# Performance work log

Hardware: AMD Instinct MI355X
Metric: run time of the kernel (lower is better)

## Reference

```python
import jax, jax.numpy as jnp
import numpy as np

# Standard NF4 quantization codebook (bitsandbytes values)
_NF4_CB = np.array([
    -1.0, -0.6961928009986877, -0.5250730514526367, -0.39491748809814453,
    -0.28444138169288635, -0.18477343022823334, -0.09105003625154495, 0.0,
    0.07958029955625534, 0.16093020141124725, 0.24611230194568634, 0.33791524171829224,
    0.44070982933044434, 0.5626170039176941, 0.7229568362236023, 1.0], dtype=np.float32)

B, L, H, E, DFF = 2, 2048, 2048, 8, 8192
BLK = 512  # NF4 quantization block size (b_idx = h // 512 in kernel)


def setup_inputs() -> dict:
    key = jax.random.key(0)
    ks = jax.random.split(key, 8)
    N = B * L
    x = jax.random.normal(ks[0], (B, L, H), dtype=jnp.float32)
    router_w = jax.random.normal(ks[1], (H, E), dtype=jnp.float32) * 0.02
    # packed NF4: one byte = two 4-bit codebook indices (low nibble -> even h)
    nf4 = jax.random.randint(ks[2], (N, E, H // 2), 0, 256, dtype=jnp.int32)
    mean = jax.random.normal(ks[3], (N, E, H // BLK), dtype=jnp.float32) * 0.01
    std = jax.random.uniform(ks[4], (N, E, H // BLK), dtype=jnp.float32) + 0.5
    codebook = jnp.asarray(_NF4_CB)
    w1 = jax.random.normal(ks[5], (H, DFF), dtype=jnp.float32) * 0.02
    w2 = jax.random.normal(ks[6], (DFF, H), dtype=jnp.float32) * 0.02
    return {"x": x, "router_w": router_w, "nf4": nf4, "mean": mean,
            "std": std, "codebook": codebook, "w1": w1, "w2": w2}


def reference(x, router_w, nf4, mean, std, codebook, w1, w2):
    b, l, h = x.shape
    n = b * l
    e = router_w.shape[1]
    xf = x.reshape(n, h)

    # shared expert MLP (base_mlp): Linear -> GELU -> Linear
    mlp = jax.nn.gelu(xf @ w1) @ w2  # [N, H]

    # router: logits in fp32, softmax, cast to fp16 as the kernel does
    logits = xf @ router_w  # [N, E]
    probs = jax.nn.softmax(logits, axis=-1).astype(jnp.float16).astype(jnp.float32)

    # NF4 unpack: low nibble -> even h, high nibble -> odd h
    low = nf4 & 15
    high = (nf4 >> 4) & 15
    idx = jnp.stack([low, high], axis=-1).reshape(n, e, h)  # interleave -> [N,E,H]
    vals = codebook[idx]  # codebook gather, [N,E,H]

    # per-block (512) rescale: val*std + mean
    nb = mean.shape[-1]
    blk = h // nb
    dq = (vals.reshape(n, e, nb, blk) * std[..., None] + mean[..., None]).reshape(n, e, h)

    # weighted expert mix + MLP residual add
    moe = jnp.einsum('ne,neh->nh', probs, dq)
    return (moe + mlp).reshape(b, l, h)
```

## Files before the change

### kernel.cpp

```cpp
#include <hip/hip_runtime.h>
#include <hip/hip_bf16.h>
#include <hip/hip_fp16.h>

#define H 2048
#define E 8
#define DFF 8192
#define NTOK 4096
#define NB 4

typedef _Float16 f16x8 __attribute__((ext_vector_type(8)));
typedef _Float16 f16x2 __attribute__((ext_vector_type(2)));
typedef float f32x4 __attribute__((ext_vector_type(4)));

#define AS1 __attribute__((address_space(1)))
#define AS3 __attribute__((address_space(3)))

__device__ __forceinline__ void gl_lds16(const void* g, void* l) {
    __builtin_amdgcn_global_load_lds((const AS1 unsigned int*)g,
                                     (AS3 unsigned int*)l, 16, 0, 0);
}

__device__ __forceinline__ float gelu_f(float x) {
    float u = 0.7978845608028654f * x * (1.0f + 0.044715f * x * x);
    float t = fabsf(u);
    float e = __expf(-2.0f * t);
    float th = (1.0f - e) / (1.0f + e);
    th = copysignf(th, u);
    return 0.5f * x * (1.0f + th);
}

__global__ __launch_bounds__(256) void router_moe_kernel(
    const float* __restrict__ x, const float* __restrict__ rw,
    const int* __restrict__ nf4, const float* __restrict__ mean,
    const float* __restrict__ stdv, const float* __restrict__ cb,
    _Float16* __restrict__ xh, float* __restrict__ moe)
{
    int n = blockIdx.x, t = threadIdx.x;
    __shared__ float red[4][E];
    __shared__ float pr[E];
    __shared__ float cbl[32];
    __shared__ float ps[E][NB];
    __shared__ float cmean[NB];

    float acc[E];
#pragma unroll
    for (int e = 0; e < E; ++e) acc[e] = 0.f;
    const float* xr = x + (size_t)n * H;
#pragma unroll
    for (int k = 0; k < H / 256; ++k) {
        int h = t + k * 256;
        float xv = xr[h];
        xh[(size_t)n * H + h] = (_Float16)xv;
        const float4* r4 = reinterpret_cast<const float4*>(rw + (size_t)h * E);
        float4 a = r4[0], b = r4[1];
        acc[0] += xv * a.x; acc[1] += xv * a.y; acc[2] += xv * a.z; acc[3] += xv * a.w;
        acc[4] += xv * b.x; acc[5] += xv * b.y; acc[6] += xv * b.z; acc[7] += xv * b.w;
    }
#pragma unroll
    for (int e = 0; e < E; ++e) {
        float v = acc[e];
#pragma unroll
        for (int o = 32; o > 0; o >>= 1) v += __shfl_down(v, o, 64);
        acc[e] = v;
    }
    int wave = t >> 6, lane = t & 63;
    if (lane == 0) {
#pragma unroll
        for (int e = 0; e < E; ++e) red[wave][e] = acc[e];
    }
    __syncthreads();
    if (t == 0) {
        float lg[E];
        float mx = -1e30f;
#pragma unroll
        for (int e = 0; e < E; ++e) {
            lg[e] = red[0][e] + red[1][e] + red[2][e] + red[3][e];
            mx = fmaxf(mx, lg[e]);
        }
        float s = 0.f;
#pragma unroll
        for (int e = 0; e < E; ++e) { lg[e] = expf(lg[e] - mx); s += lg[e]; }
        float inv = 1.f / s;
#pragma unroll
        for (int e = 0; e < E; ++e) {
            float p = lg[e] * inv;
            pr[e] = __half2float(__float2half(p));
        }
    }
    __syncthreads();

    if (t < 16) { float v = cb[t]; cbl[t] = v; cbl[t + 16] = v; }
    else if (t >= 32 && t < 64) {
        int e = (t - 32) >> 2, b = t & 3;
        ps[e][b] = pr[e] * stdv[((size_t)n * E + e) * NB + b];
    } else if (t >= 64 && t < 68) {
        int b = t - 64; float s = 0.f;
        for (int e = 0; e < E; ++e)
            s += pr[e] * mean[((size_t)n * E + e) * NB + b];
        cmean[b] = s;
    }
    __syncthreads();

    int b = t >> 6;
    int cboff = (t & 1) << 4;
    const int4* w4 = reinterpret_cast<const int4*>(nf4 + (size_t)n * (E * H / 2));
    float o[8];
    float cm = cmean[b];
#pragma unroll
    for (int u = 0; u < 8; ++u) o[u] = cm;
#pragma unroll
    for (int e = 0; e < E; ++e) {
        int4 wv = w4[e * 256 + t];
        float pse = ps[e][b];
        int w0 = wv.x, w1 = wv.y, w2 = wv.z, w3 = wv.w;
        o[0] += pse * cbl[(w0 & 15) + cboff];
        o[1] += pse * cbl[((w0 >> 4) & 15) + cboff];
        o[2] += pse * cbl[(w1 & 15) + cboff];
        o[3] += pse * cbl[((w1 >> 4) & 15) + cboff];
        o[4] += pse * cbl[(w2 & 15) + cboff];
        o[5] += pse * cbl[((w2 >> 4) & 15) + cboff];
        o[6] += pse * cbl[(w3 & 15) + cboff];
        o[7] += pse * cbl[((w3 >> 4) & 15) + cboff];
    }
    float4* op = reinterpret_cast<float4*>(moe + (size_t)n * H + 8 * t);
    op[0] = make_float4(o[0], o[1], o[2], o[3]);
    op[1] = make_float4(o[4], o[5], o[6], o[7]);
}

__global__ __launch_bounds__(256) void transpose_cast_kernel(
    const float* __restrict__ src, _Float16* __restrict__ dst, int R, int C)
{
    __shared__ float tile[64][65];
    int t = threadIdx.x;
    int c0 = blockIdx.x * 64, r0 = blockIdx.y * 64;
    int ct = (t & 15) * 4, rt = t >> 4;
#pragma unroll
    for (int i = 0; i < 4; ++i) {
        int r = rt + i * 16;
        float4 v = *reinterpret_cast<const float4*>(src + (size_t)(r0 + r) * C + c0 + ct);
        tile[r][ct] = v.x; tile[r][ct + 1] = v.y;
        tile[r][ct + 2] = v.z; tile[r][ct + 3] = v.w;
    }
    __syncthreads();
    int u = (t & 31) * 2, cq = t >> 5;
#pragma unroll
    for (int i = 0; i < 8; ++i) {
        int c = cq + i * 8;
        f16x2 pk;
        pk[0] = (_Float16)tile[u][c];
        pk[1] = (_Float16)tile[u + 1][c];
        *reinterpret_cast<f16x2*>(dst + (size_t)(c0 + c) * R + r0 + u) = pk;
    }
}

template <int EPI, int MAP>
__global__ __launch_bounds__(512, 2) void gemm5b_kernel(
    const _Float16* __restrict__ A, const _Float16* __restrict__ Bt,
    const float* __restrict__ addsrc, void* __restrict__ outv,
    float* __restrict__ aux, int K, int LDK, int N)
{
    __shared__ uint4 lds_u4[163840 / 16];
    char* lds = (char*)lds_u4;

    int t = threadIdx.x;
    int id = blockIdx.x;
    int xcd = id & 7, chunk = id >> 3;
    int by, bx, ks = 0;
    if constexpr (MAP == 0) {
        by = (xcd & 1) * 8 + (chunk & 7);
        bx = (xcd >> 1) * 8 + (chunk >> 3);
    } else {
        by = (xcd >> 1) * 4 + (chunk & 3);
        bx = (xcd & 1) * 4 + ((chunk >> 2) & 3);
        ks = chunk >> 4;
    }
    int m0 = by * 256, n0 = bx * 256;
    int koff = ks * K;

    const unsigned short* sA = (const unsigned short*)A
        + (size_t)(m0 + (t & 255)) * LDK + koff + (t >> 8) * 8;
    const unsigned short* sB = (const unsigned short*)Bt
        + (size_t)(n0 + (t & 255)) * LDK + koff + (t >> 8) * 8;
    unsigned dstT = (unsigned)t * 16;

    int lane = t & 63, wave = t >> 6;
    int wr = wave >> 2, wc = wave & 3;
    int mb = wr * 128, nb = wc * 64;
    int q = lane >> 4, m16 = lane & 15;

    unsigned aOff = (unsigned)(q * 4096 + (mb + m16) * 16);
    unsigned bOff = (unsigned)(16384 + q * 4096 + (nb + m16) * 16);

    f32x4 acc[8][4] = {};
    f16x8 afL[4], afH[4], bf[4];

#define STG_A(Wb, T) do { \
    gl_lds16(sA + (size_t)(T) * 32,      (Wb) + dstT); \
    gl_lds16(sA + (size_t)(T) * 32 + 16, (Wb) + 8192 + dstT); } while (0)
#define STG_B(Wb, T) do { \
    gl_lds16(sB + (size_t)(T) * 32,      (Wb) + 16384 + dstT); \
    gl_lds16(sB + (size_t)(T) * 32 + 16, (Wb) + 16384 + 8192 + dstT); } while (0)
#define RD_B(Rb) do { \
    _Pragma("unroll") for (int jl = 0; jl < 4; ++jl) \
        bf[jl] = *(const f16x8*)((Rb) + bOff + jl * 256); } while (0)
#define RD_AL(Rb) do { \
    _Pragma("unroll") for (int il = 0; il < 4; ++il) \
        afL[il] = *(const f16x8*)((Rb) + aOff + il * 256); } while (0)
#define RD_AH(Rb) do { \
    _Pragma("unroll") for (int il = 0; il < 4; ++il) \
        afH[il] = *(const f16x8*)((Rb) + aOff + 1024 + il * 256); } while (0)
#define MM(i0, afr) do { \
    __builtin_amdgcn_s_setprio(1); \
    _Pragma("unroll") for (int il = 0; il < 4; ++il) \
    _Pragma("unroll") for (int jl = 0; jl < 4; ++jl) \
        acc[(i0) + il][jl] = __builtin_amdgcn_mfma_f32_16x16x32_f16( \
            afr[il], bf[jl], acc[(i0) + il][jl], 0, 0, 0); \
    __builtin_amdgcn_s_setprio(0); } while (0)
#define BARR  asm volatile("s_barrier" ::: "memory")
#define LGKM0 asm volatile("s_waitcnt lgkmcnt(0)" ::: "memory")

    STG_A(lds,         0); STG_B(lds,         0);
    STG_A(lds + 32768, 1); STG_B(lds + 32768, 1);
    STG_A(lds + 65536, 2); STG_B(lds + 65536, 2);
    asm volatile("s_waitcnt vmcnt(8)" ::: "memory");
    BARR;

    int NT = K / 32;
    unsigned rb = 0, wb = 3 * 32768;
    for (int T = 0; T < NT; ++T) {
        char* R = lds + rb;
        char* W = lds + wb;
        bool st = (T + 3 < NT);

        RD_B(R); RD_AL(R);
        if (st) STG_A(W, T + 3);
        BARR; LGKM0;
        MM(0, afL);
        BARR;
        RD_AH(R);
        if (st) STG_B(W, T + 3);
        BARR; LGKM0;
        MM(4, afH);
        if (st) asm volatile("s_waitcnt vmcnt(8)" ::: "memory");
        else    asm volatile("s_waitcnt vmcnt(0)" ::: "memory");
        BARR;

        rb += 32768; if (rb == 163840) rb = 0;
        wb += 32768; if (wb == 163840) wb = 0;
    }

#pragma unroll
    for (int i = 0; i < 8; ++i)
#pragma unroll
        for (int j = 0; j < 4; ++j) {
            int row = m0 + mb + i * 16 + q * 4;
            int col = n0 + nb + j * 16 + m16;
#pragma unroll
            for (int rix = 0; rix < 4; ++rix) {
                float v = acc[i][j][rix];
                size_t o = (size_t)(row + rix) * N + col;
                if constexpr (EPI == 0) {
                    ((_Float16*)outv)[o] = (_Float16)gelu_f(v);
                } else {
                    if (ks == 0) ((float*)outv)[o] = v + addsrc[o];
                    else         aux[o] = v;
                }
            }
        }
#undef STG_A
#undef STG_B
#undef RD_B
#undef RD_AL
#undef RD_AH
#undef MM
#undef BARR
#undef LGKM0
}

__global__ __launch_bounds__(256) void combine_kernel(
    float* __restrict__ out, const float* __restrict__ part)
{
    size_t base = (size_t)blockIdx.x * 256 + threadIdx.x;
    const float4* p4 = (const float4*)part;
    float4* o4 = (float4*)out;
#pragma unroll
    for (int s = 0; s < 4; ++s) {
        size_t i = base + (size_t)s * 524288;
        float4 a = o4[i], b = p4[i];
        o4[i] = make_float4(a.x + b.x, a.y + b.y, a.z + b.z, a.w + b.w);
    }
}

extern "C" void kernel_launch(void* const* d_in, const int* in_sizes, int n_in,
                              void* d_out, int out_size, void* d_ws, size_t ws_size,
                              hipStream_t stream) {
    const float* x    = (const float*)d_in[0];
    const float* rw   = (const float*)d_in[1];
    const int*   nf4  = (const int*)d_in[2];
    const float* mean = (const float*)d_in[3];
    const float* stdv = (const float*)d_in[4];
    const float* cb   = (const float*)d_in[5];
    const float* w1   = (const float*)d_in[6];
    const float* w2   = (const float*)d_in[7];
    float* out = (float*)d_out;

    char* ws = (char*)d_ws;
    float* moe        = (float*)(ws + 131072);
    _Float16* xh      = (_Float16*)(ws + 33685504);
    _Float16* w1t     = (_Float16*)(ws + 50462720);
    _Float16* w2t     = (_Float16*)(ws + 84017152);
    _Float16* hid     = (_Float16*)(ws + 117571584);
    float* pbuf       = (float*)(ws + 50462720);

    router_moe_kernel<<<NTOK, 256, 0, stream>>>(x, rw, nf4, mean, stdv, cb, xh, moe);
    transpose_cast_kernel<<<dim3(DFF / 64, H / 64), 256, 0, stream>>>(w1, w1t, H, DFF);
    transpose_cast_kernel<<<dim3(H / 64, DFF / 64), 256, 0, stream>>>(w2, w2t, DFF, H);
    gemm5b_kernel<0, 0><<<512, 512, 0, stream>>>(xh, w1t, nullptr, (void*)hid,
                                                 nullptr, H, H, DFF);
    gemm5b_kernel<1, 1><<<256, 512, 0, stream>>>(hid, w2t, moe, (void*)out,
                                                 pbuf, DFF / 2, DFF, H);
    combine_kernel<<<2048, 256, 0, stream>>>(out, pbuf);
}
```

Before: 724.8 us.

## Drop mid-iteration GEMM barriers and merge the two weight-transpose launches

The GEMM main loop loses its two mid-iteration s_barrier and lgkmcnt(0) waits and the s_setprio toggles around the MFMA blocks. Both A and B staging for tile T+3 are now issued up front, leaving one barrier per K-step; the 5-slot LDS ring keeps the read and write slots apart. The two transpose-cast launches are folded into one kernel that picks w1 or w2 by block index. The goal is less barrier stall and launch overhead, at the cost of letting waves drift apart and possibly worse MFMA/memory interleaving without the priority hints.

```diff
diff --git a/kernel.cpp b/kernel.cpp
--- a/kernel.cpp
+++ b/kernel.cpp
@@ -127,12 +127,23 @@
     op[1] = make_float4(o[4], o[5], o[6], o[7]);
 }
 
-__global__ __launch_bounds__(256) void transpose_cast_kernel(
-    const float* __restrict__ src, _Float16* __restrict__ dst, int R, int C)
+__global__ __launch_bounds__(256) void transpose2_kernel(
+    const float* __restrict__ w1, const float* __restrict__ w2,
+    _Float16* __restrict__ w1t, _Float16* __restrict__ w2t)
 {
     __shared__ float tile[64][65];
+    int id = blockIdx.x;
+    const float* src; _Float16* dst; int R, C, bx, by;
+    if (id < (DFF / 64) * (H / 64)) {
+        src = w1; dst = w1t; R = H; C = DFF;
+        bx = id % (DFF / 64); by = id / (DFF / 64);
+    } else {
+        id -= (DFF / 64) * (H / 64);
+        src = w2; dst = w2t; R = DFF; C = H;
+        bx = id % (H / 64); by = id / (H / 64);
+    }
     int t = threadIdx.x;
-    int c0 = blockIdx.x * 64, r0 = blockIdx.y * 64;
+    int c0 = bx * 64, r0 = by * 64;
     int ct = (t & 15) * 4, rt = t >> 4;
 #pragma unroll
     for (int i = 0; i < 4; ++i) {
@@ -154,7 +165,7 @@
 }
 
 template <int EPI, int MAP>
-__global__ __launch_bounds__(512, 2) void gemm5b_kernel(
+__global__ __launch_bounds__(512, 2) void gemmW_kernel(
     const _Float16* __restrict__ A, const _Float16* __restrict__ Bt,
     const float* __restrict__ addsrc, void* __restrict__ outv,
     float* __restrict__ aux, int K, int LDK, int N)
@@ -210,14 +221,11 @@
     _Pragma("unroll") for (int il = 0; il < 4; ++il) \
         afH[il] = *(const f16x8*)((Rb) + aOff + 1024 + il * 256); } while (0)
 #define MM(i0, afr) do { \
-    __builtin_amdgcn_s_setprio(1); \
     _Pragma("unroll") for (int il = 0; il < 4; ++il) \
     _Pragma("unroll") for (int jl = 0; jl < 4; ++jl) \
         acc[(i0) + il][jl] = __builtin_amdgcn_mfma_f32_16x16x32_f16( \
-            afr[il], bf[jl], acc[(i0) + il][jl], 0, 0, 0); \
-    __builtin_amdgcn_s_setprio(0); } while (0)
+            afr[il], bf[jl], acc[(i0) + il][jl], 0, 0, 0); } while (0)
 #define BARR  asm volatile("s_barrier" ::: "memory")
-#define LGKM0 asm volatile("s_waitcnt lgkmcnt(0)" ::: "memory")
 
     STG_A(lds,         0); STG_B(lds,         0);
     STG_A(lds + 32768, 1); STG_B(lds + 32768, 1);
@@ -232,15 +240,13 @@
         char* W = lds + wb;
         bool st = (T + 3 < NT);
 
-        RD_B(R); RD_AL(R);
-        if (st) STG_A(W, T + 3);
-        BARR; LGKM0;
+        RD_B(R);
+        RD_AL(R);
+        if (st) { STG_A(W, T + 3); STG_B(W, T + 3); }
         MM(0, afL);
-        BARR;
         RD_AH(R);
-        if (st) STG_B(W, T + 3);
-        BARR; LGKM0;
         MM(4, afH);
+
         if (st) asm volatile("s_waitcnt vmcnt(8)" ::: "memory");
         else    asm volatile("s_waitcnt vmcnt(0)" ::: "memory");
         BARR;
@@ -274,7 +280,6 @@
 #undef RD_AH
 #undef MM
 #undef BARR
-#undef LGKM0
 }
 
 __global__ __launch_bounds__(256) void combine_kernel(
@@ -313,11 +318,10 @@
     float* pbuf       = (float*)(ws + 50462720);
 
     router_moe_kernel<<<NTOK, 256, 0, stream>>>(x, rw, nf4, mean, stdv, cb, xh, moe);
-    transpose_cast_kernel<<<dim3(DFF / 64, H / 64), 256, 0, stream>>>(w1, w1t, H, DFF);
-    transpose_cast_kernel<<<dim3(H / 64, DFF / 64), 256, 0, stream>>>(w2, w2t, DFF, H);
-    gemm5b_kernel<0, 0><<<512, 512, 0, stream>>>(xh, w1t, nullptr, (void*)hid,
-                                                 nullptr, H, H, DFF);
-    gemm5b_kernel<1, 1><<<256, 512, 0, stream>>>(hid, w2t, moe, (void*)out,
-                                                 pbuf, DFF / 2, DFF, H);
+    transpose2_kernel<<<2 * (DFF / 64) * (H / 64), 256, 0, stream>>>(w1, w2, w1t, w2t);
+    gemmW_kernel<0, 0><<<512, 512, 0, stream>>>(xh, w1t, nullptr, (void*)hid,
+                                                nullptr, H, H, DFF);
+    gemmW_kernel<1, 1><<<256, 512, 0, stream>>>(hid, w2t, moe, (void*)out,
+                                                pbuf, DFF / 2, DFF, H);
     combine_kernel<<<2048, 256, 0, stream>>>(out, pbuf);
 }
```

Result: slower. 752.6 us (+3.8%).
